# Kernel tuning notes

Hardware: AMD Instinct MI355X
Metric: run time of the kernel (lower is better)

## Reference

```python
import jax, jax.numpy as jnp
import numpy as np

N_NODES = 10000
N_EDGES = 160000
NEG_SLOPE = 0.2  # PyG GATv2Conv default negative_slope


def _gatv2_layer(x, src, dst, Wl, Wr, bl, br, att, bias, heads, ch):
    """GATv2Conv (PyG semantics, share_weights=False, concat=True).
    x: [N, F_in]; src/dst: [E] (message j->i means src=j, dst=i).
    Wl/Wr: [F_in, heads*ch]; att: [heads, ch]; bias: [heads*ch].
    """
    n = x.shape[0]
    xl = (x @ Wl + bl).reshape(n, heads, ch)  # source-side transform
    xr = (x @ Wr + br).reshape(n, heads, ch)  # target-side transform
    s = xl[src] + xr[dst]                      # [E, H, C]
    s = jnp.where(s > 0, s, NEG_SLOPE * s)     # LeakyReLU
    e = jnp.einsum('ehc,hc->eh', s, att)       # [E, H] attention logits
    # segment softmax over incoming edges of each target node
    emax = jax.ops.segment_max(e, dst, num_segments=n)
    emax = jnp.where(jnp.isfinite(emax), emax, 0.0)
    ex = jnp.exp(e - emax[dst])
    denom = jax.ops.segment_sum(ex, dst, num_segments=n)
    alpha = ex / (denom[dst] + 1e-16)          # [E, H]
    out = jax.ops.segment_sum(alpha[:, :, None] * xl[src], dst, num_segments=n)
    return out.reshape(n, heads * ch) + bias


def setup_inputs() -> dict:
    key = jax.random.key(0)
    ks = jax.random.split(key, 16)
    x = jax.random.normal(ks[0], (N_NODES, 4), dtype=jnp.float32)
    edge_index = jax.random.randint(ks[1], (2, N_EDGES), 0, N_NODES, dtype=jnp.int64)

    def glorot(k, shape):
        fan_in = shape[0]
        return (jax.random.normal(k, shape, dtype=jnp.float32) / np.sqrt(fan_in)).astype(jnp.float32)

    # layer 1: in=4, heads=8, out=120 -> 960
    W1l = glorot(ks[2], (4, 960)); W1r = glorot(ks[3], (4, 960))
    b1l = jnp.zeros((960,), jnp.float32); b1r = jnp.zeros((960,), jnp.float32)
    att1 = glorot(ks[4], (8, 120))
    bias1 = jnp.zeros((960,), jnp.float32)
    # layer 2: in=960, heads=1, out=4
    W2l = glorot(ks[5], (960, 4)); W2r = glorot(ks[6], (960, 4))
    b2l = jnp.zeros((4,), jnp.float32); b2r = jnp.zeros((4,), jnp.float32)
    att2 = glorot(ks[7], (1, 4))
    bias2 = jnp.zeros((4,), jnp.float32)
    return {"x": x, "edge_index": edge_index,
            "W1l": W1l, "W1r": W1r, "b1l": b1l, "b1r": b1r, "att1": att1, "bias1": bias1,
            "W2l": W2l, "W2r": W2r, "b2l": b2l, "b2r": b2r, "att2": att2, "bias2": bias2}


def reference(x, edge_index, W1l, W1r, b1l, b1r, att1, bias1,
              W2l, W2r, b2l, b2r, att2, bias2):
    n = x.shape[0]
    loop = jnp.arange(n, dtype=edge_index.dtype)
    src = jnp.concatenate([edge_index[0], loop])  # PyG add_self_loops=True default
    dst = jnp.concatenate([edge_index[1], loop])
    h = _gatv2_layer(x, src, dst, W1l, W1r, b1l, b1r, att1, bias1, heads=8, ch=120)
    h = jax.nn.relu(h)
    # F.dropout: identity in inference/reference (deterministic baseline)
    out = _gatv2_layer(h, src, dst, W2l, W2r, b2l, b2r, att2, bias2, heads=1, ch=4)
    return out
```

## Files before the change

kernel.cpp:

```cpp
#include <hip/hip_runtime.h>

#define N_NODES 10000
#define N_EDGES 160000
#define E_TOT   170000
#define H1      8
#define C1      120
#define F1      960
#define BSTRIDE 64

typedef _Float16 h2 __attribute__((ext_vector_type(2)));
typedef _Float16 f16x8 __attribute__((ext_vector_type(8)));
typedef float f32x4 __attribute__((ext_vector_type(4)));
typedef float f32x16 __attribute__((ext_vector_type(16)));
union H2U { unsigned u; h2 h; };
union AU  { uint4 u; f16x8 h; };

#if defined(__has_builtin)
#if __has_builtin(__builtin_amdgcn_fdot2)
#define FDOT2(a,b,c) __builtin_amdgcn_fdot2((a),(b),(c),false)
#endif
#endif
#ifndef FDOT2
#define FDOT2(a,b,c) ((float)(a)[0]*(float)(b)[0] + (float)(a)[1]*(float)(b)[1] + (c))
#endif

__device__ __forceinline__ float lrelu(float v) { return fmaxf(v, 0.2f * v); }
__device__ __forceinline__ unsigned packh2(float a, float b) {
    H2U u; u.h = (h2){(_Float16)a, (_Float16)b}; return u.u;
}
__device__ __forceinline__ h2 toh2(unsigned v) { H2U u; u.u = v; return u.h; }

__global__ __launch_bounds__(256) void prep(
        const float* __restrict__ x,
        const float* __restrict__ W1l, const float* __restrict__ W1r,
        const float* __restrict__ b1l, const float* __restrict__ b1r,
        const float* __restrict__ att1, const float* __restrict__ bias1,
        const float* __restrict__ W2l, const float* __restrict__ W2r,
        uint4* __restrict__ BpH, int* __restrict__ Bh,
        uint2* __restrict__ WAh, unsigned* __restrict__ PBh,
        uint4* __restrict__ W2P,
        uint2* __restrict__ xh, float* __restrict__ Ls, float* __restrict__ Lr,
        int* __restrict__ cnt) {
    int b = blockIdx.x, t = threadIdx.x;
    if (b >= 44) {
        int i = (b - 44) * 256 + t;
        if (i < N_NODES) cnt[i] = 0;
        return;
    }
    if (b < 4) {
        BpH[b*512 + t]       = make_uint4(0u,0u,0u,0u);
        BpH[b*512 + 256 + t] = make_uint4(0u,0u,0u,0u);
        __syncthreads();
        if (t < 240) {
            int rc = b * 240 + t;
            int h = rc / C1, u = rc - h * C1;
            float a = att1[rc];
            int cntPos = 0, rankB = 0;
            for (int v = 0; v < C1; ++v) {
                bool pos = att1[h*C1 + v] > 0.f;
                cntPos += pos ? 1 : 0;
                rankB  += (v < u && pos) ? 1 : 0;
            }
            int newu = (a > 0.f) ? rankB : (cntPos + (u - rankB));
            float sc = fabsf(0.4f * a);
            float wl0 = W1l[rc], wl1 = W1l[F1+rc], wl2 = W1l[2*F1+rc], wl3 = W1l[3*F1+rc];
            float wr0 = W1r[rc], wr1 = W1r[F1+rc], wr2 = W1r[2*F1+rc], wr3 = W1r[3*F1+rc];
            float bc = b1l[rc] + b1r[rc];
            int pc2 = h * 128 + newu;
            int ct = pc2 >> 5, cl2 = pc2 & 31;
            BpH[ct*64 + cl2] = make_uint4(packh2(sc*wl0, sc*wl1), packh2(sc*wl2, sc*wl3),
                                          packh2(sc*wr0, sc*wr1), packh2(sc*wr2, sc*wr3));
            BpH[ct*64 + 32 + cl2] = make_uint4(packh2(sc*bc, 0.f), 0u, 0u, 0u);
            if (u == 0) Bh[h] = cntPos;
            WAh[rc] = make_uint2(packh2(wl0, wl1), packh2(wl2, wl3));
            PBh[rc] = packh2(b1l[rc], bias1[rc]);
        }
        if (t < 120) {
            int i = b * 120 + t;
            int h = i / 60, u = i - h * 60;
            int c0 = h * C1 + u, c1 = c0 + 60;
            const float4 wl0 = ((const float4*)W2l)[c0], wl1 = ((const float4*)W2l)[c1];
            const float4 wr0 = ((const float4*)W2r)[c0], wr1 = ((const float4*)W2r)[c1];
            W2P[i*2]   = make_uint4(packh2(wl0.x, wl1.x), packh2(wl0.y, wl1.y),
                                    packh2(wl0.z, wl1.z), packh2(wl0.w, wl1.w));
            W2P[i*2+1] = make_uint4(packh2(wr0.x, wr1.x), packh2(wr0.y, wr1.y),
                                    packh2(wr0.z, wr1.z), packh2(wr0.w, wr1.w));
        }
        return;
    }
    __shared__ float Pp[3][72];
    __shared__ float Ps[72];
    {
        int o = t % 72, p = t / 72;
        if (t < 216) {
            int h = o / 9, j = o % 9;
            float acc = 0.f;
            int u0 = p * 40;
            for (int u = u0; u < u0 + 40; ++u) {
                int c = h * C1 + u;
                float a = att1[c];
                float w;
                if (j < 4)      w = W1l[j * F1 + c];
                else if (j < 8) w = W1r[(j - 4) * F1 + c];
                else            w = b1l[c] + b1r[c];
                acc = fmaf(a, w, acc);
            }
            Pp[p][o] = acc;
        }
    }
    __syncthreads();
    if (t < 72) Ps[t] = 0.6f * (Pp[0][t] + Pp[1][t] + Pp[2][t]);
    __syncthreads();
    int n = (b - 4) * 250 + t;
    if (t < 250) {
        float4 xv = ((const float4*)x)[n];
        xh[n] = make_uint2(packh2(xv.x, xv.y), packh2(xv.z, xv.w));
#pragma unroll
        for (int h = 0; h < H1; ++h) {
            const float* p = Ps + h * 9;
            Ls[n*8+h] = xv.x*p[0] + xv.y*p[1] + xv.z*p[2] + xv.w*p[3];
            Lr[n*8+h] = xv.x*p[4] + xv.y*p[5] + xv.z*p[6] + xv.w*p[7] + p[8];
        }
    }
}


__global__ __launch_bounds__(512) void logits_mfma(
        const int* __restrict__ ei, const uint2* __restrict__ xh,
        const uint4* __restrict__ BpH, const int* __restrict__ Bh,
        const float* __restrict__ Ls, const float* __restrict__ Lr,
        int* __restrict__ cnt, int* __restrict__ slist,
        float* __restrict__ e1) {
    __shared__ uint4 BpL[2048];
    __shared__ int eposL[256];
    int tid = threadIdx.x;
#pragma unroll
    for (int i = 0; i < 4; ++i) BpL[tid + i*512] = BpH[tid + i*512];
    {
        int lidx = tid & 255;
        int ef = blockIdx.x * 256 + lidx;
        if (tid < 256 && ef < E_TOT) {
            int s, d;
            if (ef < N_EDGES) { s = ei[ef]; d = ei[N_EDGES + ef]; }
            else { s = ef - N_EDGES; d = s; }
            int pos = atomicAdd(&cnt[d], 1);
            int slot = d * BSTRIDE + pos;
            slist[slot] = s;
            eposL[lidx] = slot;
        }
    }
    __syncthreads();

    int ebase = blockIdx.x * 256 + (tid >> 6) * 32;
    if (ebase >= E_TOT) return;
    int lane = tid & 63;
    int ecol = lane & 31, g2 = lane >> 5;

    int s0 = 0, d0 = 0;
    AU zu;
    if (g2 == 0) {
        int er = ebase + ecol;
        if (er >= E_TOT) er = E_TOT - 1;
        if (er < N_EDGES) { s0 = ei[er]; d0 = ei[N_EDGES + er]; }
        else { s0 = er - N_EDGES; d0 = s0; }
        uint2 a = xh[s0], bb = xh[d0];
        zu.u = make_uint4(a.x, a.y, bb.x, bb.y);
    } else {
        zu.u = make_uint4(0x00003C00u, 0u, 0u, 0u);
    }
    int sA = __shfl(s0, ecol, 64), dA = __shfl(d0, ecol, 64);
    float4 lsv = *(const float4*)(Ls + sA*8 + 4*g2);
    float4 lrv = *(const float4*)(Lr + dA*8 + 4*g2);

    float kk0 = 0.f, kk1 = 0.f, kk2 = 0.f, kk3 = 0.f;
#pragma unroll
    for (int h = 0; h < H1; ++h) {
        int bh = Bh[h];
        float aa = 0.f;
#pragma unroll
        for (int tt = 0; tt < 4; ++tt) {
            int ct = h * 4 + tt;
            AU wu; wu.u = BpL[ct*64 + lane];
            f32x16 z = {0.f,0.f,0.f,0.f,0.f,0.f,0.f,0.f,0.f,0.f,0.f,0.f,0.f,0.f,0.f,0.f};
            f32x16 dd = __builtin_amdgcn_mfma_f32_32x32x16_f16(wu.h, zu.h, z, 0, 0, 0);
#pragma unroll
            for (int r = 0; r < 16; ++r) {
                int row = (r & 3) + 8 * (r >> 2) + 4 * g2;
                float sel = (tt*32 + row < bh) ? 1.f : -1.f;
                aa = fmaf(sel, fabsf(dd[r]), aa);
            }
        }
        aa += __shfl_xor(aa, 32, 64);
        bool pk = ((h >> 2) == g2);
        if ((h & 3) == 0)      kk0 = pk ? aa : kk0;
        else if ((h & 3) == 1) kk1 = pk ? aa : kk1;
        else if ((h & 3) == 2) kk2 = pk ? aa : kk2;
        else                   kk3 = pk ? aa : kk3;
    }

    {
        int e0 = ebase + ecol;
        if (e0 < E_TOT) {
            int slot = eposL[(tid >> 6) * 32 + ecol];
            float4 o = make_float4(__expf(lsv.x + lrv.x + kk0),
                                   __expf(lsv.y + lrv.y + kk1),
                                   __expf(lsv.z + lrv.z + kk2),
                                   __expf(lsv.w + lrv.w + kk3));
            *(float4*)(e1 + (size_t)slot*8 + 4*g2) = o;
        }
    }
}


#define AGG(hi, wv) { float W_ = (wv); ssum[hi] += W_; ag[hi].x += W_*xv.x; ag[hi].y += W_*xv.y; ag[hi].z += W_*xv.z; ag[hi].w += W_*xv.w; }

__global__ __launch_bounds__(256) void fused_agg1(
        const int* __restrict__ cnt, const int* __restrict__ slist,
        const float* __restrict__ e1, const float* __restrict__ x,
        const uint2* __restrict__ WAh, const unsigned* __restrict__ PBh,
        const uint4* __restrict__ W2P,
        const float* __restrict__ b2l, const float* __restrict__ b2r,
        float* __restrict__ xl2, float* __restrict__ xr2) {
    int tid = threadIdx.x;
    int node = blockIdx.x * 16 + (tid >> 4);
    int l = tid & 15;
    int beg = node * BSTRIDE, end = beg + cnt[node];

    float ssum[H1]; float4 ag[H1];
#pragma unroll
    for (int h = 0; h < H1; ++h) { ssum[h] = 0.f; ag[h] = make_float4(0.f,0.f,0.f,0.f); }

    for (int i = beg + l; i < end; i += 16) {
        const float4* p = (const float4*)(e1 + (size_t)i * 8);
        float4 wa = p[0], wb = p[1];
        float4 xv = ((const float4*)x)[slist[i]];
        AGG(0, wa.x) AGG(1, wa.y) AGG(2, wa.z) AGG(3, wa.w)
        AGG(4, wb.x) AGG(5, wb.y) AGG(6, wb.z) AGG(7, wb.w)
    }
#pragma unroll
    for (int off = 8; off; off >>= 1) {
#pragma unroll
        for (int h = 0; h < H1; ++h) {
            ssum[h] += __shfl_xor(ssum[h], off, 64);
            ag[h].x += __shfl_xor(ag[h].x, off, 64);
            ag[h].y += __shfl_xor(ag[h].y, off, 64);
            ag[h].z += __shfl_xor(ag[h].z, off, 64);
            ag[h].w += __shfl_xor(ag[h].w, off, 64);
        }
    }
    unsigned agA[H1], agB[H1], sg[H1];
#pragma unroll
    for (int h = 0; h < H1; ++h) {
        float inv = 1.f / (ssum[h] + 1e-16f);
        agA[h] = packh2(ag[h].x * inv, ag[h].y * inv);
        agB[h] = packh2(ag[h].z * inv, ag[h].w * inv);
        sg[h]  = packh2(ssum[h] * inv, 1.f);
    }

    float al0=0, al1=0, al2=0, al3=0, ar0=0, ar1=0, ar2=0, ar3=0;
#pragma unroll
    for (int h = 0; h < H1; ++h) {
        h2 ga = toh2(agA[h]), gb = toh2(agB[h]), gs = toh2(sg[h]);
#pragma unroll
        for (int j = 0; j < 4; ++j) {
            int u = l + 16*j;
            if (u < 60) {
                int c0 = h*C1 + u;
                uint2 wa0 = WAh[c0];      unsigned pb0 = PBh[c0];
                uint2 wa1 = WAh[c0 + 60]; unsigned pb1 = PBh[c0 + 60];
                float f0 = FDOT2(gs, toh2(pb0), 0.f);
                f0 = FDOT2(ga, toh2(wa0.x), f0);
                f0 = FDOT2(gb, toh2(wa0.y), f0);
                f0 = fmaxf(f0, 0.f);
                float f1 = FDOT2(gs, toh2(pb1), 0.f);
                f1 = FDOT2(ga, toh2(wa1.x), f1);
                f1 = FDOT2(gb, toh2(wa1.y), f1);
                f1 = fmaxf(f1, 0.f);
                h2 hp = toh2(packh2(f0, f1));
                int pi = (h*60 + u) * 2;
                uint4 wA = W2P[pi], wB = W2P[pi + 1];
                al0 = FDOT2(hp, toh2(wA.x), al0); al1 = FDOT2(hp, toh2(wA.y), al1);
                al2 = FDOT2(hp, toh2(wA.z), al2); al3 = FDOT2(hp, toh2(wA.w), al3);
                ar0 = FDOT2(hp, toh2(wB.x), ar0); ar1 = FDOT2(hp, toh2(wB.y), ar1);
                ar2 = FDOT2(hp, toh2(wB.z), ar2); ar3 = FDOT2(hp, toh2(wB.w), ar3);
            }
        }
    }
#pragma unroll
    for (int off = 8; off; off >>= 1) {
        al0 += __shfl_xor(al0, off, 64); al1 += __shfl_xor(al1, off, 64);
        al2 += __shfl_xor(al2, off, 64); al3 += __shfl_xor(al3, off, 64);
        ar0 += __shfl_xor(ar0, off, 64); ar1 += __shfl_xor(ar1, off, 64);
        ar2 += __shfl_xor(ar2, off, 64); ar3 += __shfl_xor(ar3, off, 64);
    }
    if (l == 0) {
        ((float4*)xl2)[node] = make_float4(al0 + b2l[0], al1 + b2l[1], al2 + b2l[2], al3 + b2l[3]);
        ((float4*)xr2)[node] = make_float4(ar0 + b2r[0], ar1 + b2r[1], ar2 + b2r[2], ar3 + b2r[3]);
    }
}


__global__ __launch_bounds__(256) void attn2(
        const int* __restrict__ cnt, const int* __restrict__ slist,
        const float* __restrict__ xl2, const float* __restrict__ xr2,
        const float* __restrict__ att2, const float* __restrict__ bias2,
        float* __restrict__ out) {
    int tid = threadIdx.x;
    int node = blockIdx.x * 16 + (tid >> 4);
    int l = tid & 15;
    int beg = node * BSTRIDE, end = beg + cnt[node];
    float4 xr = ((const float4*)xr2)[node];
    float a0 = att2[0], a1 = att2[1], a2 = att2[2], a3 = att2[3];

    float ssum = 0.f;
    float4 acc = make_float4(0.f, 0.f, 0.f, 0.f);
    for (int i = beg + l; i < end; i += 16) {
        float4 v = ((const float4*)xl2)[slist[i]];
        float lg = a0*lrelu(v.x + xr.x) + a1*lrelu(v.y + xr.y)
                 + a2*lrelu(v.z + xr.z) + a3*lrelu(v.w + xr.w);
        float w = __expf(lg);
        ssum += w;
        acc.x += w*v.x; acc.y += w*v.y; acc.z += w*v.z; acc.w += w*v.w;
    }
#pragma unroll
    for (int off = 8; off; off >>= 1) {
        ssum  += __shfl_xor(ssum,  off, 64);
        acc.x += __shfl_xor(acc.x, off, 64);
        acc.y += __shfl_xor(acc.y, off, 64);
        acc.z += __shfl_xor(acc.z, off, 64);
        acc.w += __shfl_xor(acc.w, off, 64);
    }
    if (l == 0) {
        float inv = 1.f / (ssum + 1e-16f);
        ((float4*)out)[node] = make_float4(acc.x*inv + bias2[0], acc.y*inv + bias2[1],
                                           acc.z*inv + bias2[2], acc.w*inv + bias2[3]);
    }
}

extern "C" void kernel_launch(void* const* d_in, const int* in_sizes, int n_in,
                              void* d_out, int out_size, void* d_ws, size_t ws_size,
                              hipStream_t stream) {
    const float* x     = (const float*)d_in[0];
    const int*   ei    = (const int*)  d_in[1];
    const float* W1l   = (const float*)d_in[2];
    const float* W1r   = (const float*)d_in[3];
    const float* b1l   = (const float*)d_in[4];
    const float* b1r   = (const float*)d_in[5];
    const float* att1  = (const float*)d_in[6];
    const float* bias1 = (const float*)d_in[7];
    const float* W2l   = (const float*)d_in[8];
    const float* W2r   = (const float*)d_in[9];
    const float* b2l   = (const float*)d_in[10];
    const float* b2r   = (const float*)d_in[11];
    const float* att2  = (const float*)d_in[12];
    const float* bias2 = (const float*)d_in[13];
    float* out = (float*)d_out;

    float* e1   = (float*)d_ws;
    float* Ls   = e1 + (size_t)N_NODES * BSTRIDE * 8;
    float* Lr   = Ls + 80000;
    float* xl2  = Lr + 80000;
    float* xr2  = xl2 + 40000;
    unsigned* BpHu = (unsigned*)(xr2 + 40000);
    int* Bh     = (int*)(BpHu + 8192);
    unsigned* WAhu = (unsigned*)(Bh + 16);
    unsigned* W2Pu = WAhu + 1920;
    unsigned* PBhu = W2Pu + 7680;
    unsigned* xhu  = PBhu + 960;
    int* cnt    = (int*)(xhu + 20000);
    int* slist  = cnt + 10000;

    const int B = 256;

    prep<<<84, B, 0, stream>>>(
        x, W1l, W1r, b1l, b1r, att1, bias1, W2l, W2r,
        (uint4*)BpHu, Bh, (uint2*)WAhu, PBhu, (uint4*)W2Pu,
        (uint2*)xhu, Ls, Lr, cnt);

    logits_mfma<<<(E_TOT + 255) / 256, 512, 0, stream>>>(
        ei, (const uint2*)xhu, (const uint4*)BpHu, Bh, Ls, Lr,
        cnt, slist, e1);
    fused_agg1<<<N_NODES / 16, B, 0, stream>>>(
        cnt, slist, e1, x, (const uint2*)WAhu, PBhu, (const uint4*)W2Pu,
        b2l, b2r, xl2, xr2);
    attn2<<<N_NODES / 16, B, 0, stream>>>(cnt, slist, xl2, xr2, att2, bias2, out);
}
```

Measured before the change: 66.12 us.

## Fold weight preprocessing and per-node linear logits into the logits kernel

Moves construction of the permuted fp16 MFMA weight tiles, the positive-count table and the 72 linear-term coefficients into every block of the logits kernel, computed straight into shared memory. Per-node Ls/Lr and packed xh are no longer precomputed: each edge reads raw x for source and destination and evaluates the linear terms inline. The prep kernel shrinks to a small aux kernel that zeroes counters and packs layer-2 weights. This removes a dependency on node-wide precompute and its global traffic, but every block now redundantly runs the O(120) rank loops and the 72 coefficient reductions serially over 32 threads.

```diff
diff --git a/kernel.cpp b/kernel.cpp
--- a/kernel.cpp
+++ b/kernel.cpp
@@ -30,29 +30,73 @@
 }
 __device__ __forceinline__ h2 toh2(unsigned v) { H2U u; u.u = v; return u.h; }
 
-__global__ __launch_bounds__(256) void prep(
-        const float* __restrict__ x,
+__global__ __launch_bounds__(256) void aux(
+        const float* __restrict__ W1l,
+        const float* __restrict__ b1l, const float* __restrict__ bias1,
+        const float* __restrict__ W2l, const float* __restrict__ W2r,
+        uint2* __restrict__ WAh, unsigned* __restrict__ PBh,
+        uint4* __restrict__ W2P, int* __restrict__ cnt) {
+    int b = blockIdx.x, t = threadIdx.x;
+    if (b < 40) {
+        int i = b * 256 + t;
+        if (i < N_NODES) cnt[i] = 0;
+        return;
+    }
+    int bb = b - 40;
+    if (t < 240) {
+        int rc = bb * 240 + t;
+        float wl0 = W1l[rc], wl1 = W1l[F1+rc], wl2 = W1l[2*F1+rc], wl3 = W1l[3*F1+rc];
+        WAh[rc] = make_uint2(packh2(wl0, wl1), packh2(wl2, wl3));
+        PBh[rc] = packh2(b1l[rc], bias1[rc]);
+    }
+    if (t < 120) {
+        int i = bb * 120 + t;
+        int h = i / 60, u = i - h * 60;
+        int c0 = h * C1 + u, c1 = c0 + 60;
+        const float4 wl0 = ((const float4*)W2l)[c0], wl1 = ((const float4*)W2l)[c1];
+        const float4 wr0 = ((const float4*)W2r)[c0], wr1 = ((const float4*)W2r)[c1];
+        W2P[i*2]   = make_uint4(packh2(wl0.x, wl1.x), packh2(wl0.y, wl1.y),
+                                packh2(wl0.z, wl1.z), packh2(wl0.w, wl1.w));
+        W2P[i*2+1] = make_uint4(packh2(wr0.x, wr1.x), packh2(wr0.y, wr1.y),
+                                packh2(wr0.z, wr1.z), packh2(wr0.w, wr1.w));
+    }
+}
+
+
+__global__ __launch_bounds__(512) void logits_all(
+        const int* __restrict__ ei, const float* __restrict__ x,
         const float* __restrict__ W1l, const float* __restrict__ W1r,
         const float* __restrict__ b1l, const float* __restrict__ b1r,
-        const float* __restrict__ att1, const float* __restrict__ bias1,
-        const float* __restrict__ W2l, const float* __restrict__ W2r,
-        uint4* __restrict__ BpH, int* __restrict__ Bh,
-        uint2* __restrict__ WAh, unsigned* __restrict__ PBh,
-        uint4* __restrict__ W2P,
-        uint2* __restrict__ xh, float* __restrict__ Ls, float* __restrict__ Lr,
-        int* __restrict__ cnt) {
-    int b = blockIdx.x, t = threadIdx.x;
-    if (b >= 44) {
-        int i = (b - 44) * 256 + t;
-        if (i < N_NODES) cnt[i] = 0;
-        return;
-    }
-    if (b < 4) {
-        BpH[b*512 + t]       = make_uint4(0u,0u,0u,0u);
-        BpH[b*512 + 256 + t] = make_uint4(0u,0u,0u,0u);
-        __syncthreads();
-        if (t < 240) {
-            int rc = b * 240 + t;
+        const float* __restrict__ att1,
+        int* __restrict__ cnt, int* __restrict__ slist,
+        float* __restrict__ e1) {
+    __shared__ uint4 BpL[2048];
+    __shared__ float PsL[72];
+    __shared__ int   BhL[8];
+    __shared__ int   eposL[256];
+    int tid = threadIdx.x;
+
+    {
+        int lidx = tid & 255;
+        int ef = blockIdx.x * 256 + lidx;
+        if (tid < 256 && ef < E_TOT) {
+            int s, d;
+            if (ef < N_EDGES) { s = ei[ef]; d = ei[N_EDGES + ef]; }
+            else { s = ef - N_EDGES; d = s; }
+            int pos = atomicAdd(&cnt[d], 1);
+            int slot = d * BSTRIDE + pos;
+            slist[slot] = s;
+            eposL[lidx] = slot;
+        }
+    }
+#pragma unroll
+    for (int i = 0; i < 4; ++i) BpL[tid + i*512] = make_uint4(0u,0u,0u,0u);
+    __syncthreads();
+
+    if (tid < 480) {
+#pragma unroll
+        for (int k = 0; k < 2; ++k) {
+            int rc = tid * 2 + k;
             int h = rc / C1, u = rc - h * C1;
             float a = att1[rc];
             int cntPos = 0, rankB = 0;
@@ -68,35 +112,16 @@
             float bc = b1l[rc] + b1r[rc];
             int pc2 = h * 128 + newu;
             int ct = pc2 >> 5, cl2 = pc2 & 31;
-            BpH[ct*64 + cl2] = make_uint4(packh2(sc*wl0, sc*wl1), packh2(sc*wl2, sc*wl3),
+            BpL[ct*64 + cl2] = make_uint4(packh2(sc*wl0, sc*wl1), packh2(sc*wl2, sc*wl3),
                                           packh2(sc*wr0, sc*wr1), packh2(sc*wr2, sc*wr3));
-            BpH[ct*64 + 32 + cl2] = make_uint4(packh2(sc*bc, 0.f), 0u, 0u, 0u);
-            if (u == 0) Bh[h] = cntPos;
-            WAh[rc] = make_uint2(packh2(wl0, wl1), packh2(wl2, wl3));
-            PBh[rc] = packh2(b1l[rc], bias1[rc]);
-        }
-        if (t < 120) {
-            int i = b * 120 + t;
-            int h = i / 60, u = i - h * 60;
-            int c0 = h * C1 + u, c1 = c0 + 60;
-            const float4 wl0 = ((const float4*)W2l)[c0], wl1 = ((const float4*)W2l)[c1];
-            const float4 wr0 = ((const float4*)W2r)[c0], wr1 = ((const float4*)W2r)[c1];
-            W2P[i*2]   = make_uint4(packh2(wl0.x, wl1.x), packh2(wl0.y, wl1.y),
-                                    packh2(wl0.z, wl1.z), packh2(wl0.w, wl1.w));
-            W2P[i*2+1] = make_uint4(packh2(wr0.x, wr1.x), packh2(wr0.y, wr1.y),
-                                    packh2(wr0.z, wr1.z), packh2(wr0.w, wr1.w));
-        }
-        return;
-    }
-    __shared__ float Pp[3][72];
-    __shared__ float Ps[72];
-    {
-        int o = t % 72, p = t / 72;
-        if (t < 216) {
+            BpL[ct*64 + 32 + cl2] = make_uint4(packh2(sc*bc, 0.f), 0u, 0u, 0u);
+            if (u == 0) BhL[h] = cntPos;
+        }
+    } else {
+        for (int o = tid - 480; o < 72; o += 32) {
             int h = o / 9, j = o % 9;
             float acc = 0.f;
-            int u0 = p * 40;
-            for (int u = u0; u < u0 + 40; ++u) {
+            for (int u = 0; u < C1; ++u) {
                 int c = h * C1 + u;
                 float a = att1[c];
                 float w;
@@ -105,48 +130,7 @@
                 else            w = b1l[c] + b1r[c];
                 acc = fmaf(a, w, acc);
             }
-            Pp[p][o] = acc;
-        }
-    }
-    __syncthreads();
-    if (t < 72) Ps[t] = 0.6f * (Pp[0][t] + Pp[1][t] + Pp[2][t]);
-    __syncthreads();
-    int n = (b - 4) * 250 + t;
-    if (t < 250) {
-        float4 xv = ((const float4*)x)[n];
-        xh[n] = make_uint2(packh2(xv.x, xv.y), packh2(xv.z, xv.w));
-#pragma unroll
-        for (int h = 0; h < H1; ++h) {
-            const float* p = Ps + h * 9;
-            Ls[n*8+h] = xv.x*p[0] + xv.y*p[1] + xv.z*p[2] + xv.w*p[3];
-            Lr[n*8+h] = xv.x*p[4] + xv.y*p[5] + xv.z*p[6] + xv.w*p[7] + p[8];
-        }
-    }
-}
-
-
-__global__ __launch_bounds__(512) void logits_mfma(
-        const int* __restrict__ ei, const uint2* __restrict__ xh,
-        const uint4* __restrict__ BpH, const int* __restrict__ Bh,
-        const float* __restrict__ Ls, const float* __restrict__ Lr,
-        int* __restrict__ cnt, int* __restrict__ slist,
-        float* __restrict__ e1) {
-    __shared__ uint4 BpL[2048];
-    __shared__ int eposL[256];
-    int tid = threadIdx.x;
-#pragma unroll
-    for (int i = 0; i < 4; ++i) BpL[tid + i*512] = BpH[tid + i*512];
-    {
-        int lidx = tid & 255;
-        int ef = blockIdx.x * 256 + lidx;
-        if (tid < 256 && ef < E_TOT) {
-            int s, d;
-            if (ef < N_EDGES) { s = ei[ef]; d = ei[N_EDGES + ef]; }
-            else { s = ef - N_EDGES; d = s; }
-            int pos = atomicAdd(&cnt[d], 1);
-            int slot = d * BSTRIDE + pos;
-            slist[slot] = s;
-            eposL[lidx] = slot;
+            PsL[o] = 0.6f * acc;
         }
     }
     __syncthreads();
@@ -157,25 +141,41 @@
     int ecol = lane & 31, g2 = lane >> 5;
 
     int s0 = 0, d0 = 0;
+    float4 xs = make_float4(0.f,0.f,0.f,0.f), xd = xs;
     AU zu;
     if (g2 == 0) {
         int er = ebase + ecol;
         if (er >= E_TOT) er = E_TOT - 1;
         if (er < N_EDGES) { s0 = ei[er]; d0 = ei[N_EDGES + er]; }
         else { s0 = er - N_EDGES; d0 = s0; }
-        uint2 a = xh[s0], bb = xh[d0];
-        zu.u = make_uint4(a.x, a.y, bb.x, bb.y);
+        xs = ((const float4*)x)[s0];
+        xd = ((const float4*)x)[d0];
+        zu.u = make_uint4(packh2(xs.x, xs.y), packh2(xs.z, xs.w),
+                          packh2(xd.x, xd.y), packh2(xd.z, xd.w));
     } else {
         zu.u = make_uint4(0x00003C00u, 0u, 0u, 0u);
     }
-    int sA = __shfl(s0, ecol, 64), dA = __shfl(d0, ecol, 64);
-    float4 lsv = *(const float4*)(Ls + sA*8 + 4*g2);
-    float4 lrv = *(const float4*)(Lr + dA*8 + 4*g2);
+    float xsx = __shfl(xs.x, ecol, 64), xsy = __shfl(xs.y, ecol, 64);
+    float xsz = __shfl(xs.z, ecol, 64), xsw = __shfl(xs.w, ecol, 64);
+    float xdx = __shfl(xd.x, ecol, 64), xdy = __shfl(xd.y, ecol, 64);
+    float xdz = __shfl(xd.z, ecol, 64), xdw = __shfl(xd.w, ecol, 64);
+    float lin0, lin1, lin2, lin3;
+    {
+        int hb = 4 * g2;
+        const float* p0 = PsL + (hb+0)*9;
+        const float* p1 = PsL + (hb+1)*9;
+        const float* p2 = PsL + (hb+2)*9;
+        const float* p3 = PsL + (hb+3)*9;
+        lin0 = xsx*p0[0]+xsy*p0[1]+xsz*p0[2]+xsw*p0[3] + xdx*p0[4]+xdy*p0[5]+xdz*p0[6]+xdw*p0[7] + p0[8];
+        lin1 = xsx*p1[0]+xsy*p1[1]+xsz*p1[2]+xsw*p1[3] + xdx*p1[4]+xdy*p1[5]+xdz*p1[6]+xdw*p1[7] + p1[8];
+        lin2 = xsx*p2[0]+xsy*p2[1]+xsz*p2[2]+xsw*p2[3] + xdx*p2[4]+xdy*p2[5]+xdz*p2[6]+xdw*p2[7] + p2[8];
+        lin3 = xsx*p3[0]+xsy*p3[1]+xsz*p3[2]+xsw*p3[3] + xdx*p3[4]+xdy*p3[5]+xdz*p3[6]+xdw*p3[7] + p3[8];
+    }
 
     float kk0 = 0.f, kk1 = 0.f, kk2 = 0.f, kk3 = 0.f;
 #pragma unroll
     for (int h = 0; h < H1; ++h) {
-        int bh = Bh[h];
+        int bh = BhL[h];
         float aa = 0.f;
 #pragma unroll
         for (int tt = 0; tt < 4; ++tt) {
@@ -202,10 +202,8 @@
         int e0 = ebase + ecol;
         if (e0 < E_TOT) {
             int slot = eposL[(tid >> 6) * 32 + ecol];
-            float4 o = make_float4(__expf(lsv.x + lrv.x + kk0),
-                                   __expf(lsv.y + lrv.y + kk1),
-                                   __expf(lsv.z + lrv.z + kk2),
-                                   __expf(lsv.w + lrv.w + kk3));
+            float4 o = make_float4(__expf(lin0 + kk0), __expf(lin1 + kk1),
+                                   __expf(lin2 + kk2), __expf(lin3 + kk3));
             *(float4*)(e1 + (size_t)slot*8 + 4*g2) = o;
         }
     }
@@ -357,29 +355,21 @@
     float* out = (float*)d_out;
 
     float* e1   = (float*)d_ws;
-    float* Ls   = e1 + (size_t)N_NODES * BSTRIDE * 8;
-    float* Lr   = Ls + 80000;
-    float* xl2  = Lr + 80000;
+    float* xl2  = e1 + (size_t)N_NODES * BSTRIDE * 8;
     float* xr2  = xl2 + 40000;
-    unsigned* BpHu = (unsigned*)(xr2 + 40000);
-    int* Bh     = (int*)(BpHu + 8192);
-    unsigned* WAhu = (unsigned*)(Bh + 16);
+    unsigned* WAhu = (unsigned*)(xr2 + 40000);
     unsigned* W2Pu = WAhu + 1920;
     unsigned* PBhu = W2Pu + 7680;
-    unsigned* xhu  = PBhu + 960;
-    int* cnt    = (int*)(xhu + 20000);
+    int* cnt    = (int*)(PBhu + 960);
     int* slist  = cnt + 10000;
 
     const int B = 256;
 
-    prep<<<84, B, 0, stream>>>(
-        x, W1l, W1r, b1l, b1r, att1, bias1, W2l, W2r,
-        (uint4*)BpHu, Bh, (uint2*)WAhu, PBhu, (uint4*)W2Pu,
-        (uint2*)xhu, Ls, Lr, cnt);
-
-    logits_mfma<<<(E_TOT + 255) / 256, 512, 0, stream>>>(
-        ei, (const uint2*)xhu, (const uint4*)BpHu, Bh, Ls, Lr,
-        cnt, slist, e1);
+    aux<<<44, B, 0, stream>>>(W1l, b1l, bias1, W2l, W2r,
+                              (uint2*)WAhu, PBhu, (uint4*)W2Pu, cnt);
+
+    logits_all<<<(E_TOT + 255) / 256, 512, 0, stream>>>(
+        ei, x, W1l, W1r, b1l, b1r, att1, cnt, slist, e1);
     fused_agg1<<<N_NODES / 16, B, 0, stream>>>(
         cnt, slist, e1, x, (const uint2*)WAhu, PBhu, (const uint4*)W2Pu,
         b2l, b2r, xl2, xr2);
```

New measurement: 167.2 us. 2.53x slower.
